# Kernel optimization log

Measured on AMD Instinct MI355X. Metric: run time of the kernel, lower is better.

Reference implementation:

```python
import jax, jax.numpy as jnp
import numpy as np

N_NODES = 50000
N_EDGES = 400000
D_IN, D_HID, D_LAT = 1024, 512, 256


def setup_inputs() -> dict:
    key = jax.random.key(0)
    k = jax.random.split(key, 6)
    x = jax.random.normal(k[0], (N_NODES, D_IN), dtype=jnp.float32)
    edge_index = jax.random.randint(k[1], (2, N_EDGES), 0, N_NODES, dtype=jnp.int32)
    # normalized adjacency weights (e.g., D^-1/2 A D^-1/2 values), positive
    edge_weight = jax.random.uniform(k[2], (N_EDGES,), dtype=jnp.float32)
    # Glorot-style init as in GCNConv.reset_parameters
    W1 = jax.random.normal(k[3], (D_IN, D_HID), dtype=jnp.float32) * (1.0 / np.sqrt(D_IN))
    b1 = jnp.zeros((D_HID,), dtype=jnp.float32)
    W2 = jax.random.normal(k[4], (D_HID, D_LAT), dtype=jnp.float32) * (1.0 / np.sqrt(D_HID))
    b2 = jnp.zeros((D_LAT,), dtype=jnp.float32)
    return {"x": x, "edge_index": edge_index, "edge_weight": edge_weight,
            "W1": W1, "b1": b1, "W2": W2, "b2": b2}


def _gcn_layer(h, src, dst, w, W, b):
    # GCNConv: spmm(adj, h @ W) + b
    s = h @ W                                   # [N, D_out] dense GEMM
    msg = s[src] * w[:, None]                   # [E, D_out] gather + scale
    agg = jax.ops.segment_sum(msg, dst, num_segments=N_NODES)  # scatter-add
    return agg + b


def reference(x, edge_index, edge_weight, W1, b1, W2, b2):
    # eval mode: F.dropout(training=False) is identity
    src, dst = edge_index[0], edge_index[1]
    h = jax.nn.relu(_gcn_layer(x, src, dst, edge_weight, W1, b1))
    out = jax.nn.relu(_gcn_layer(h, src, dst, edge_weight, W2, b2))
    return out
```

## Files before the change

kernel.cpp:

```cpp
#include <hip/hip_runtime.h>

typedef __attribute__((ext_vector_type(8))) short short8;
typedef __attribute__((ext_vector_type(4))) float floatx4;

#define GLOBAL_AS __attribute__((address_space(1)))
#define LDS_AS __attribute__((address_space(3)))

__device__ __forceinline__ void gload_lds16(const void* g, void* l) {
  __builtin_amdgcn_global_load_lds((const GLOBAL_AS unsigned int*)g,
                                   (LDS_AS unsigned int*)l, 16, 0, 0);
}

__device__ __forceinline__ unsigned short rnbf(float f) {
  unsigned int v = __builtin_bit_cast(unsigned int, f);
  return (unsigned short)((v + 0x7fff + ((v >> 16) & 1)) >> 16);
}
__device__ __forceinline__ float bflo(unsigned int u) {
  return __builtin_bit_cast(float, u << 16);
}
__device__ __forceinline__ float bfhi(unsigned int u) {
  return __builtin_bit_cast(float, u & 0xffff0000u);
}

#define TM 128
#define TN 128
#define BKE 64

__global__ __launch_bounds__(256) void gemm_bf16(
    const unsigned short* __restrict__ A,
    const unsigned short* __restrict__ Bt,
    unsigned short* __restrict__ C,
    int M, int N, int K) {
  __shared__ __align__(16) unsigned short As[TM * BKE];
  __shared__ __align__(16) unsigned short Bs[TN * BKE];

  const int tid  = threadIdx.x;
  const int wave = tid >> 6;
  const int lane = tid & 63;
  const int wm = wave >> 1, wn = wave & 1;
  const int l15 = lane & 15, quad = lane >> 4;

  const int bm = blockIdx.y * TM;
  const int bn = blockIdx.x * TN;

  floatx4 acc[4][4];
#pragma unroll
  for (int i = 0; i < 4; ++i)
#pragma unroll
    for (int j = 0; j < 4; ++j) acc[i][j] = (floatx4){0.f, 0.f, 0.f, 0.f};

  const unsigned short* aptr[4];
  const unsigned short* bptr[4];
  int ldsoff[4];
#pragma unroll
  for (int j = 0; j < 4; ++j) {
    int ci = (wave * 4 + j) * 64 + lane;
    int r  = ci >> 3;
    int cs = (ci & 7) ^ (r & 7);
    int arow = bm + r; if (arow >= M) arow = M - 1;
    aptr[j] = A  + (size_t)arow * K + cs * 8;
    bptr[j] = Bt + (size_t)(bn + r) * K + cs * 8;
    ldsoff[j] = (wave * 4 + j) * 64 * 8;
  }

  for (int k0 = 0; k0 < K; k0 += BKE) {
#pragma unroll
    for (int j = 0; j < 4; ++j) {
      gload_lds16(aptr[j] + k0, &As[ldsoff[j]]);
      gload_lds16(bptr[j] + k0, &Bs[ldsoff[j]]);
    }
    __syncthreads();
#pragma unroll
    for (int s = 0; s < 2; ++s) {
      short8 af[4], bf[4];
#pragma unroll
      for (int mt = 0; mt < 4; ++mt) {
        int mrow = wm * 64 + mt * 16 + l15;
        int sw = (s * 4 + quad) ^ (mrow & 7);
        af[mt] = *(const short8*)&As[(mrow * 8 + sw) * 8];
      }
#pragma unroll
      for (int nt = 0; nt < 4; ++nt) {
        int nrow = wn * 64 + nt * 16 + l15;
        int sw = (s * 4 + quad) ^ (nrow & 7);
        bf[nt] = *(const short8*)&Bs[(nrow * 8 + sw) * 8];
      }
#pragma unroll
      for (int mt = 0; mt < 4; ++mt)
#pragma unroll
        for (int nt = 0; nt < 4; ++nt)
          acc[mt][nt] = __builtin_amdgcn_mfma_f32_16x16x32_bf16(
              af[mt], bf[nt], acc[mt][nt], 0, 0, 0);
    }
    __syncthreads();
  }

#pragma unroll
  for (int mt = 0; mt < 4; ++mt) {
#pragma unroll
    for (int nt = 0; nt < 4; ++nt) {
      const int col = bn + wn * 64 + nt * 16 + l15;
#pragma unroll
      for (int i = 0; i < 4; ++i) {
        const int row = bm + wm * 64 + mt * 16 + quad * 4 + i;
        if (row < M) C[(size_t)row * N + col] = rnbf(acc[mt][nt][i]);
      }
    }
  }
}

__global__ __launch_bounds__(256) void cast_f32_to_bf16(
    const float* __restrict__ in, unsigned short* __restrict__ out,
    long long n4) {
  long long i = (long long)blockIdx.x * 256 + threadIdx.x;
  if (i >= n4) return;
  float4 v = ((const float4*)in)[i];
  ushort4 o;
  o.x = rnbf(v.x); o.y = rnbf(v.y); o.z = rnbf(v.z); o.w = rnbf(v.w);
  ((ushort4*)out)[i] = o;
}

__global__ __launch_bounds__(256) void transpose_cast_bf16(
    const float* __restrict__ in, unsigned short* __restrict__ out,
    int K, int N) {
  __shared__ float t[32][33];
  const int bx = blockIdx.x * 32;
  const int by = blockIdx.y * 32;
  const int tx = threadIdx.x & 31, ty = threadIdx.x >> 5;
#pragma unroll
  for (int j = 0; j < 4; ++j)
    t[ty + j * 8][tx] = in[(size_t)(by + ty + j * 8) * N + bx + tx];
  __syncthreads();
#pragma unroll
  for (int j = 0; j < 4; ++j)
    out[(size_t)(bx + ty + j * 8) * K + by + tx] = rnbf(t[tx][ty + j * 8]);
}

__global__ __launch_bounds__(256) void hist_dst(
    const int* __restrict__ dst, int* __restrict__ cnt, int E) {
  int e = blockIdx.x * blockDim.x + threadIdx.x;
  if (e < E) atomicAdd(&cnt[dst[e]], 1);
}

__global__ __launch_bounds__(1024) void scan_csr(
    int* __restrict__ cursor, int* __restrict__ rowptr, int n) {
  __shared__ int wsum[16];
  __shared__ int carry_s;
  const int t = threadIdx.x;
  const int wv = t >> 6, ln = t & 63;
  if (t == 0) carry_s = 0;
  __syncthreads();
  for (int base = 0; base < n; base += 1024) {
    const int i = base + t;
    const int v = (i < n) ? cursor[i] : 0;
    int x = v;
#pragma unroll
    for (int off = 1; off < 64; off <<= 1) {
      int y = __shfl_up(x, off, 64);
      if (ln >= off) x += y;
    }
    if (ln == 63) wsum[wv] = x;
    __syncthreads();
    if (t < 16) {
      int s = wsum[t];
#pragma unroll
      for (int off = 1; off < 16; off <<= 1) {
        int y = __shfl_up(s, off, 64);
        if (t >= off) s += y;
      }
      wsum[t] = s;
    }
    __syncthreads();
    const int prev  = (wv > 0) ? wsum[wv - 1] : 0;
    const int inc   = x + prev;
    const int carry = carry_s;
    if (i < n) {
      rowptr[i + 1] = carry + inc;
      cursor[i]     = carry + inc - v;
    }
    __syncthreads();
    if (t == 1023) carry_s = carry + inc;
  }
  if (t == 0) rowptr[0] = 0;
}

__global__ __launch_bounds__(256) void fill_csr(
    const int* __restrict__ dst, const int* __restrict__ src,
    const float* __restrict__ w, int* __restrict__ cursor,
    int* __restrict__ es, float* __restrict__ ws, int E) {
  int e = blockIdx.x * blockDim.x + threadIdx.x;
  if (e < E) {
    int pos = atomicAdd(&cursor[dst[e]], 1);
    es[pos] = src[e];
    ws[pos] = w[e];
  }
}

__global__ __launch_bounds__(256) void gather1_b2b(
    const unsigned short* __restrict__ S, const int* __restrict__ es,
    const float* __restrict__ ws, const int* __restrict__ rowptr,
    const float* __restrict__ bias, unsigned short* __restrict__ out, int Nn) {
  const int tn = threadIdx.x & 63;
  const int node = blockIdx.x * 4 + (threadIdx.x >> 6);
  if (node >= Nn) return;
  const int f = tn << 3;
  float acc[8] = {};
  const int beg = rowptr[node], end = rowptr[node + 1];
  for (int b = beg; b < end; b += 64) {
    const int m = end - b;
    int   sv_l = 0;
    float w_l  = 0.f;
    if (tn < m) { sv_l = es[b + tn]; w_l = ws[b + tn]; }
    const int cnt = (m < 64) ? m : 64;
    for (int i = 0; i < cnt; ++i) {
      const int   sv = __shfl(sv_l, i, 64);
      const float ww = __shfl(w_l, i, 64);
      const uint4 u = *(const uint4*)(S + (size_t)sv * 512 + f);
      acc[0] = fmaf(bflo(u.x), ww, acc[0]);
      acc[1] = fmaf(bfhi(u.x), ww, acc[1]);
      acc[2] = fmaf(bflo(u.y), ww, acc[2]);
      acc[3] = fmaf(bfhi(u.y), ww, acc[3]);
      acc[4] = fmaf(bflo(u.z), ww, acc[4]);
      acc[5] = fmaf(bfhi(u.z), ww, acc[5]);
      acc[6] = fmaf(bflo(u.w), ww, acc[6]);
      acc[7] = fmaf(bfhi(u.w), ww, acc[7]);
    }
  }
  float r[8];
#pragma unroll
  for (int j = 0; j < 8; ++j) r[j] = fmaxf(acc[j] + bias[f + j], 0.f);
  uint4 o;
  o.x = (unsigned int)rnbf(r[0]) | ((unsigned int)rnbf(r[1]) << 16);
  o.y = (unsigned int)rnbf(r[2]) | ((unsigned int)rnbf(r[3]) << 16);
  o.z = (unsigned int)rnbf(r[4]) | ((unsigned int)rnbf(r[5]) << 16);
  o.w = (unsigned int)rnbf(r[6]) | ((unsigned int)rnbf(r[7]) << 16);
  *(uint4*)(out + (size_t)node * 512 + f) = o;
}

__global__ __launch_bounds__(256) void gather2_b2f(
    const unsigned short* __restrict__ S, const int* __restrict__ es,
    const float* __restrict__ ws, const int* __restrict__ rowptr,
    const float* __restrict__ bias, float* __restrict__ out, int Nn) {
  const int tn = threadIdx.x & 31;
  const int node = blockIdx.x * 8 + (threadIdx.x >> 5);
  if (node >= Nn) return;
  const int f = tn << 3;
  float acc[8] = {};
  const int beg = rowptr[node], end = rowptr[node + 1];
  for (int b = beg; b < end; b += 32) {
    const int m = end - b;
    int   sv_l = 0;
    float w_l  = 0.f;
    if (tn < m) { sv_l = es[b + tn]; w_l = ws[b + tn]; }
    const int cnt = (m < 32) ? m : 32;
    for (int i = 0; i < cnt; ++i) {
      const int   sv = __shfl(sv_l, i, 32);
      const float ww = __shfl(w_l, i, 32);
      const uint4 u = *(const uint4*)(S + (size_t)sv * 256 + f);
      acc[0] = fmaf(bflo(u.x), ww, acc[0]);
      acc[1] = fmaf(bfhi(u.x), ww, acc[1]);
      acc[2] = fmaf(bflo(u.y), ww, acc[2]);
      acc[3] = fmaf(bfhi(u.y), ww, acc[3]);
      acc[4] = fmaf(bflo(u.z), ww, acc[4]);
      acc[5] = fmaf(bfhi(u.z), ww, acc[5]);
      acc[6] = fmaf(bflo(u.w), ww, acc[6]);
      acc[7] = fmaf(bfhi(u.w), ww, acc[7]);
    }
  }
  float4 o1, o2;
  o1.x = fmaxf(acc[0] + bias[f + 0], 0.f);
  o1.y = fmaxf(acc[1] + bias[f + 1], 0.f);
  o1.z = fmaxf(acc[2] + bias[f + 2], 0.f);
  o1.w = fmaxf(acc[3] + bias[f + 3], 0.f);
  o2.x = fmaxf(acc[4] + bias[f + 4], 0.f);
  o2.y = fmaxf(acc[5] + bias[f + 5], 0.f);
  o2.z = fmaxf(acc[6] + bias[f + 6], 0.f);
  o2.w = fmaxf(acc[7] + bias[f + 7], 0.f);
  *(float4*)(out + (size_t)node * 256 + f) = o1;
  *(float4*)(out + (size_t)node * 256 + f + 4) = o2;
}

extern "C" void kernel_launch(void* const* d_in, const int* in_sizes, int n_in,
                              void* d_out, int out_size, void* d_ws, size_t ws_size,
                              hipStream_t stream) {
  const float* x  = (const float*)d_in[0];
  const int*   ei = (const int*)d_in[1];
  const float* ew = (const float*)d_in[2];
  const float* W1 = (const float*)d_in[3];
  const float* b1 = (const float*)d_in[4];
  const float* W2 = (const float*)d_in[5];
  const float* b2 = (const float*)d_in[6];

  const int D_IN = 1024, D_HID = 512, D_LAT = 256;
  const int Nn = in_sizes[0] / D_IN;
  const int E  = in_sizes[2];
  const int* src  = ei;
  const int* dstp = ei + E;

  char* base = (char*)d_ws;
  const size_t szA = (size_t)Nn * D_IN * 2;
  const size_t szB = (size_t)Nn * D_HID * 2;
  unsigned short* xb  = (unsigned short*)base;
  unsigned short* hb  = (unsigned short*)base;
  unsigned short* s1  = (unsigned short*)(base + szA);
  unsigned short* s2  = (unsigned short*)(base + szA);
  char* tail = base + szA + szB;
  unsigned short* W1t = (unsigned short*)tail;
  unsigned short* W2t = W1t + (size_t)D_IN * D_HID;
  int*   rowptr = (int*)(W2t + (size_t)D_HID * D_LAT);
  int*   cursor = rowptr + (Nn + 1);
  int*   es     = cursor + Nn;
  float* wsrt   = (float*)(es + E);

  hipMemsetAsync(cursor, 0, (size_t)Nn * sizeof(int), stream);
  hist_dst<<<(E + 255) / 256, 256, 0, stream>>>(dstp, cursor, E);
  scan_csr<<<1, 1024, 0, stream>>>(cursor, rowptr, Nn);
  fill_csr<<<(E + 255) / 256, 256, 0, stream>>>(dstp, src, ew, cursor, es, wsrt, E);

  long long n4 = (long long)Nn * D_IN / 4;
  cast_f32_to_bf16<<<(int)((n4 + 255) / 256), 256, 0, stream>>>(x, xb, n4);
  transpose_cast_bf16<<<dim3(D_HID / 32, D_IN / 32), 256, 0, stream>>>(
      W1, W1t, D_IN, D_HID);
  transpose_cast_bf16<<<dim3(D_LAT / 32, D_HID / 32), 256, 0, stream>>>(
      W2, W2t, D_HID, D_LAT);

  dim3 g1(D_HID / TN, (Nn + TM - 1) / TM);
  gemm_bf16<<<g1, 256, 0, stream>>>(xb, W1t, s1, Nn, D_HID, D_IN);
  gather1_b2b<<<(Nn + 3) / 4, 256, 0, stream>>>(
      s1, es, wsrt, rowptr, b1, hb, Nn);

  dim3 g2(D_LAT / TN, (Nn + TM - 1) / TM);
  gemm_bf16<<<g2, 256, 0, stream>>>(hb, W2t, s2, Nn, D_LAT, D_HID);
  gather2_b2f<<<(Nn + 7) / 8, 256, 0, stream>>>(
      s2, es, wsrt, rowptr, b2, (float*)d_out, Nn);
}
```

Measured before the change: 605.2 us.

## Fuse preprocessing into one cooperative kernel and remap GEMM tiles per XCD

Result: slower. 1.142 ms (+88.6%).

```diff
diff --git a/kernel.cpp b/kernel.cpp
--- a/kernel.cpp
+++ b/kernel.cpp
@@ -1,4 +1,7 @@
 #include <hip/hip_runtime.h>
+#include <hip/hip_cooperative_groups.h>
+
+namespace cg = cooperative_groups;
 
 typedef __attribute__((ext_vector_type(8))) short short8;
 typedef __attribute__((ext_vector_type(4))) float floatx4;
@@ -40,8 +43,13 @@
   const int wm = wave >> 1, wn = wave & 1;
   const int l15 = lane & 15, quad = lane >> 4;
 
-  const int bm = blockIdx.y * TM;
-  const int bn = blockIdx.x * TN;
+  const int nwg = gridDim.x * gridDim.y;
+  const int bid = blockIdx.y * gridDim.x + blockIdx.x;
+  const int q = nwg >> 3, r = nwg & 7;
+  const int xcd = bid & 7, off = bid >> 3;
+  const int lid = ((xcd < r) ? xcd * (q + 1) : r * (q + 1) + (xcd - r) * q) + off;
+  const int bm = (lid / gridDim.x) * TM;
+  const int bn = (lid % gridDim.x) * TN;
 
   floatx4 acc[4][4];
 #pragma unroll
@@ -55,11 +63,11 @@
 #pragma unroll
   for (int j = 0; j < 4; ++j) {
     int ci = (wave * 4 + j) * 64 + lane;
-    int r  = ci >> 3;
-    int cs = (ci & 7) ^ (r & 7);
-    int arow = bm + r; if (arow >= M) arow = M - 1;
+    int rr = ci >> 3;
+    int cs = (ci & 7) ^ (rr & 7);
+    int arow = bm + rr; if (arow >= M) arow = M - 1;
     aptr[j] = A  + (size_t)arow * K + cs * 8;
-    bptr[j] = Bt + (size_t)(bn + r) * K + cs * 8;
+    bptr[j] = Bt + (size_t)(bn + rr) * K + cs * 8;
     ldsoff[j] = (wave * 4 + j) * 64 * 8;
   }
 
@@ -109,90 +117,126 @@
   }
 }
 
-__global__ __launch_bounds__(256) void cast_f32_to_bf16(
-    const float* __restrict__ in, unsigned short* __restrict__ out,
-    long long n4) {
-  long long i = (long long)blockIdx.x * 256 + threadIdx.x;
-  if (i >= n4) return;
-  float4 v = ((const float4*)in)[i];
-  ushort4 o;
-  o.x = rnbf(v.x); o.y = rnbf(v.y); o.z = rnbf(v.z); o.w = rnbf(v.w);
-  ((ushort4*)out)[i] = o;
-}
-
-__global__ __launch_bounds__(256) void transpose_cast_bf16(
-    const float* __restrict__ in, unsigned short* __restrict__ out,
-    int K, int N) {
-  __shared__ float t[32][33];
-  const int bx = blockIdx.x * 32;
-  const int by = blockIdx.y * 32;
-  const int tx = threadIdx.x & 31, ty = threadIdx.x >> 5;
-#pragma unroll
-  for (int j = 0; j < 4; ++j)
-    t[ty + j * 8][tx] = in[(size_t)(by + ty + j * 8) * N + bx + tx];
-  __syncthreads();
-#pragma unroll
-  for (int j = 0; j < 4; ++j)
-    out[(size_t)(bx + ty + j * 8) * K + by + tx] = rnbf(t[tx][ty + j * 8]);
-}
-
-__global__ __launch_bounds__(256) void hist_dst(
-    const int* __restrict__ dst, int* __restrict__ cnt, int E) {
-  int e = blockIdx.x * blockDim.x + threadIdx.x;
-  if (e < E) atomicAdd(&cnt[dst[e]], 1);
-}
-
-__global__ __launch_bounds__(1024) void scan_csr(
-    int* __restrict__ cursor, int* __restrict__ rowptr, int n) {
-  __shared__ int wsum[16];
-  __shared__ int carry_s;
-  const int t = threadIdx.x;
-  const int wv = t >> 6, ln = t & 63;
-  if (t == 0) carry_s = 0;
-  __syncthreads();
-  for (int base = 0; base < n; base += 1024) {
-    const int i = base + t;
-    const int v = (i < n) ? cursor[i] : 0;
-    int x = v;
-#pragma unroll
-    for (int off = 1; off < 64; off <<= 1) {
-      int y = __shfl_up(x, off, 64);
-      if (ln >= off) x += y;
-    }
-    if (ln == 63) wsum[wv] = x;
-    __syncthreads();
-    if (t < 16) {
-      int s = wsum[t];
-#pragma unroll
-      for (int off = 1; off < 16; off <<= 1) {
-        int y = __shfl_up(s, off, 64);
-        if (t >= off) s += y;
-      }
-      wsum[t] = s;
-    }
-    __syncthreads();
-    const int prev  = (wv > 0) ? wsum[wv - 1] : 0;
-    const int inc   = x + prev;
-    const int carry = carry_s;
-    if (i < n) {
-      rowptr[i + 1] = carry + inc;
-      cursor[i]     = carry + inc - v;
-    }
-    __syncthreads();
-    if (t == 1023) carry_s = carry + inc;
-  }
-  if (t == 0) rowptr[0] = 0;
-}
-
-__global__ __launch_bounds__(256) void fill_csr(
-    const int* __restrict__ dst, const int* __restrict__ src,
-    const float* __restrict__ w, int* __restrict__ cursor,
-    int* __restrict__ es, float* __restrict__ ws, int E) {
-  int e = blockIdx.x * blockDim.x + threadIdx.x;
-  if (e < E) {
-    int pos = atomicAdd(&cursor[dst[e]], 1);
-    es[pos] = src[e];
-    ws[pos] = w[e];
+#define NB 1024
+#define NT 256
+
+__global__ __launch_bounds__(256, 4) void prep_fused(
+    const float* __restrict__ x, const float* __restrict__ W1,
+    const float* __restrict__ W2, const int* __restrict__ src,
+    const int* __restrict__ dst, const float* __restrict__ ew,
+    unsigned short* __restrict__ xb, unsigned short* __restrict__ W1t,
+    unsigned short* __restrict__ W2t, int* __restrict__ rowptr,
+    int* __restrict__ cursor, int* __restrict__ es, float* __restrict__ ws,
+    int* __restrict__ partials, int Nn, int E) {
+  cg::grid_group grid = cg::this_grid();
+  const int b = blockIdx.x, t = threadIdx.x;
+  const int tx = t & 31, ty = t >> 5;
+  __shared__ float tile[32][33];
+  __shared__ int sred[8];
+
+  if (b < 512) {
+    const int bx = (b & 15) * 32, by = (b >> 4) * 32;
+#pragma unroll
+    for (int j = 0; j < 4; ++j)
+      tile[ty + j * 8][tx] = W1[(size_t)(by + ty + j * 8) * 512 + bx + tx];
+    __syncthreads();
+#pragma unroll
+    for (int j = 0; j < 4; ++j)
+      W1t[(size_t)(bx + ty + j * 8) * 1024 + by + tx] = rnbf(tile[tx][ty + j * 8]);
+  } else if (b < 640) {
+    const int id = b - 512;
+    const int bx = (id & 7) * 32, by = (id >> 3) * 32;
+#pragma unroll
+    for (int j = 0; j < 4; ++j)
+      tile[ty + j * 8][tx] = W2[(size_t)(by + ty + j * 8) * 256 + bx + tx];
+    __syncthreads();
+#pragma unroll
+    for (int j = 0; j < 4; ++j)
+      W2t[(size_t)(bx + ty + j * 8) * 512 + by + tx] = rnbf(tile[tx][ty + j * 8]);
+  } else if (b < 840) {
+    const int i = (b - 640) * NT + t;
+    if (i < Nn) cursor[i] = 0;
+  }
+  grid.sync();
+
+  const long long n4 = (long long)Nn * 1024 / 4;
+  const long long half = n4 / 2;
+  if (b < 512) {
+    for (int e = b * NT + t; e < E; e += 512 * NT) atomicAdd(&cursor[dst[e]], 1);
+  } else {
+    for (long long i = (long long)(b - 512) * NT + t; i < half; i += 512LL * NT) {
+      float4 v = ((const float4*)x)[i];
+      ushort4 o;
+      o.x = rnbf(v.x); o.y = rnbf(v.y); o.z = rnbf(v.z); o.w = rnbf(v.w);
+      ((ushort4*)xb)[i] = o;
+    }
+  }
+  grid.sync();
+
+  const int Cn = (Nn + NB - 1) / NB;
+  if (t < 64) {
+    const int idx = b * Cn + t;
+    const int v = (t < Cn && idx < Nn) ? cursor[idx] : 0;
+    int xs = v;
+#pragma unroll
+    for (int o = 1; o < 64; o <<= 1) {
+      int y = __shfl_up(xs, o, 64);
+      if (t >= o) xs += y;
+    }
+    if (t < Cn && idx < Nn) rowptr[idx + 1] = xs;
+    if (t == 63) partials[b] = xs;
+  }
+  grid.sync();
+
+  if (b == 0) {
+    const int p0 = partials[t * 4], p1 = partials[t * 4 + 1];
+    const int p2 = partials[t * 4 + 2], p3 = partials[t * 4 + 3];
+    const int ssum = p0 + p1 + p2 + p3;
+    int xs = ssum;
+    const int ln = t & 63, wv = t >> 6;
+#pragma unroll
+    for (int o = 1; o < 64; o <<= 1) {
+      int y = __shfl_up(xs, o, 64);
+      if (ln >= o) xs += y;
+    }
+    if (ln == 63) sred[wv] = xs;
+    __syncthreads();
+    int wpre = 0;
+    for (int k = 0; k < wv; ++k) wpre += sred[k];
+    const int exc = wpre + xs - ssum;
+    partials[t * 4]     = exc;
+    partials[t * 4 + 1] = exc + p0;
+    partials[t * 4 + 2] = exc + p0 + p1;
+    partials[t * 4 + 3] = exc + p0 + p1 + p2;
+  }
+  grid.sync();
+
+  if (t < Cn) {
+    const int idx = b * Cn + t;
+    if (idx < Nn) {
+      const int v = cursor[idx];
+      const int inc = partials[b] + rowptr[idx + 1];
+      rowptr[idx + 1] = inc;
+      cursor[idx] = inc - v;
+    }
+  }
+  if (b == 0 && t == 0) rowptr[0] = 0;
+  grid.sync();
+
+  if (b < 512) {
+    for (int e = b * NT + t; e < E; e += 512 * NT) {
+      const int pos = atomicAdd(&cursor[dst[e]], 1);
+      es[pos] = src[e];
+      ws[pos] = ew[e];
+    }
+  } else {
+    for (long long i = half + (long long)(b - 512) * NT + t; i < n4;
+         i += 512LL * NT) {
+      float4 v = ((const float4*)x)[i];
+      ushort4 o;
+      o.x = rnbf(v.x); o.y = rnbf(v.y); o.z = rnbf(v.z); o.w = rnbf(v.w);
+      ((ushort4*)xb)[i] = o;
+    }
   }
 }
 
@@ -307,22 +351,19 @@
   char* tail = base + szA + szB;
   unsigned short* W1t = (unsigned short*)tail;
   unsigned short* W2t = W1t + (size_t)D_IN * D_HID;
-  int*   rowptr = (int*)(W2t + (size_t)D_HID * D_LAT);
-  int*   cursor = rowptr + (Nn + 1);
-  int*   es     = cursor + Nn;
-  float* wsrt   = (float*)(es + E);
-
-  hipMemsetAsync(cursor, 0, (size_t)Nn * sizeof(int), stream);
-  hist_dst<<<(E + 255) / 256, 256, 0, stream>>>(dstp, cursor, E);
-  scan_csr<<<1, 1024, 0, stream>>>(cursor, rowptr, Nn);
-  fill_csr<<<(E + 255) / 256, 256, 0, stream>>>(dstp, src, ew, cursor, es, wsrt, E);
-
-  long long n4 = (long long)Nn * D_IN / 4;
-  cast_f32_to_bf16<<<(int)((n4 + 255) / 256), 256, 0, stream>>>(x, xb, n4);
-  transpose_cast_bf16<<<dim3(D_HID / 32, D_IN / 32), 256, 0, stream>>>(
-      W1, W1t, D_IN, D_HID);
-  transpose_cast_bf16<<<dim3(D_LAT / 32, D_HID / 32), 256, 0, stream>>>(
-      W2, W2t, D_HID, D_LAT);
+  int*   rowptr   = (int*)(W2t + (size_t)D_HID * D_LAT);
+  int*   cursor   = rowptr + (Nn + 1);
+  int*   es       = cursor + Nn;
+  float* wsrt     = (float*)(es + E);
+  int*   partials = (int*)(wsrt + E);
+
+  int Nn_a = Nn, E_a = E;
+  void* args[] = {(void*)&x,      (void*)&W1,   (void*)&W2,   (void*)&src,
+                  (void*)&dstp,   (void*)&ew,   (void*)&xb,   (void*)&W1t,
+                  (void*)&W2t,    (void*)&rowptr, (void*)&cursor, (void*)&es,
+                  (void*)&wsrt,   (void*)&partials, (void*)&Nn_a, (void*)&E_a};
+  hipLaunchCooperativeKernel((const void*)prep_fused, dim3(NB), dim3(NT), args,
+                             0u, stream);
 
   dim3 g1(D_HID / TN, (Nn + TM - 1) / TM);
   gemm_bf16<<<g1, 256, 0, stream>>>(xb, W1t, s1, Nn, D_HID, D_IN);
```
